# Kernel tuning notes

Measured on AMD Instinct MI355X. Metric: run time of the kernel, lower is better.

## Reference

```python
import jax, jax.numpy as jnp
from jax import lax
import numpy as np

N_NEURON = 4096
BATCH = 64
N_STEP = 200


def setup_inputs() -> dict:
    key = jax.random.key(0)
    k1, k2, k3 = jax.random.split(key, 3)
    # state_g is a sigmoid output: keep strictly inside (0, 1) for g_inverse's log
    state_g = jax.random.uniform(k1, (BATCH, N_NEURON), dtype=jnp.float32,
                                 minval=0.05, maxval=0.95)
    # Symmetric_Linear init: W ~ N(0, 0.01), symmetrized, zero diagonal
    W = jax.random.normal(k2, (N_NEURON, N_NEURON), dtype=jnp.float32) * 0.01
    W = W + W.T
    W = W - jnp.diag(jnp.diag(W))
    b = jax.random.normal(k3, (N_NEURON,), dtype=jnp.float32) * 0.01
    beta = jnp.ones((N_NEURON,), dtype=jnp.float32) * 10.0
    tau = jnp.ones((N_NEURON,), dtype=jnp.float32)
    dt_train = jnp.float32(0.1)
    return {"state_g": state_g, "W": W, "b": b, "beta": beta, "tau": tau,
            "dt_train": dt_train, "n_step": N_STEP}


def reference(state_g, W, b, beta, tau, dt_train, n_step):
    # max_x = 50 / beta.max()  (original uses .item(); beta is constant so same value)
    max_x = 50.0 / jnp.max(beta)
    # Symmetric_Linear effective weight: (W + W^T)/2 with zero diagonal.
    # Original recomputes this every step; it's step-invariant so hoist it.
    W_sym = (W + W.T) * 0.5 - jnp.diag(jnp.diag(W))
    # g_inverse: x = (1/beta) * log(g / (1 - g))
    state_x = (1.0 / beta) * jnp.log(state_g / (1.0 - state_g))
    alpha = dt_train / tau  # [N]

    def step(carry, _):
        x, g = carry
        pre = g @ W_sym.T + b                       # [B, N] GEMM
        x = alpha * pre + (1.0 - alpha) * x         # leaky update
        x = jnp.clip(x, -max_x, max_x)
        g = jax.nn.sigmoid(beta * x)
        return (x, g), None

    (state_x, state_g), _ = lax.scan(step, (state_x, state_g), None, length=n_step)
    return state_g
```

## Files before the change

### kernel.cpp

```cpp
#include <hip/hip_runtime.h>
#include <hip/hip_bf16.h>

#define MM 64
#define NN 4096
#define KK 4096
#define NSTEP 200

typedef __bf16 bf16x8 __attribute__((ext_vector_type(8)));
typedef float  f32x4  __attribute__((ext_vector_type(4)));

static __device__ __forceinline__ unsigned short f2bf(float f) {
    __hip_bfloat16 h = __float2bfloat16(f);
    return __builtin_bit_cast(unsigned short, h);
}
static __device__ __forceinline__ float bf2f(unsigned short u) {
    __hip_bfloat16 h = __builtin_bit_cast(__hip_bfloat16, u);
    return __bfloat162float(h);
}


__global__ __launch_bounds__(256) void symm_kernel(const float* __restrict__ W,
                                                   unsigned short* __restrict__ Wfh,
                                                   unsigned short* __restrict__ Wfl) {
    __shared__ float T[64][65];
    const int tid = threadIdx.x;
    const int r0 = blockIdx.y * 64, c0 = blockIdx.x * 64;
#pragma unroll
    for (int i = 0; i < 4; ++i) {
        int lin = tid + i * 256;
        int cc  = lin >> 4;
        int r4  = (lin & 15) * 4;
        float4 v = *(const float4*)&W[(size_t)(c0 + cc) * NN + r0 + r4];
        T[cc][r4 + 0] = v.x; T[cc][r4 + 1] = v.y;
        T[cc][r4 + 2] = v.z; T[cc][r4 + 3] = v.w;
    }
    __syncthreads();
#pragma unroll
    for (int i = 0; i < 4; ++i) {
        int lin = tid + i * 256;
        int rr  = lin >> 4;
        int c4  = (lin & 15) * 4;
        float4 v = *(const float4*)&W[(size_t)(r0 + rr) * NN + c0 + c4];
        float d[4] = {v.x, v.y, v.z, v.w};
        ushort4 ohi, olo;
        unsigned short* ph = (unsigned short*)&ohi;
        unsigned short* pl = (unsigned short*)&olo;
#pragma unroll
        for (int j = 0; j < 4; ++j) {
            float sv = 0.5f * (d[j] + T[c4 + j][rr]);
            if (r0 + rr == c0 + c4 + j) sv = 0.0f;
            unsigned short hi = f2bf(sv);
            ph[j] = hi;
            pl[j] = f2bf(sv - bf2f(hi));
        }
        const int n  = r0 + rr;
        const int kg = c0 + c4;
        const int s16 = n >> 4, ln = n & 15;
        const int kc = kg >> 5, q = (kg & 31) >> 3, j0 = kg & 7;
        size_t off = (((size_t)s16 * 128 + kc) * 64 + q * 16 + ln) * 8 + j0;
        *(ushort4*)&Wfh[off] = ohi;
        *(ushort4*)&Wfl[off] = olo;
    }
}

__global__ __launch_bounds__(256) void init_kernel(const float* __restrict__ g_in,
                                                   const float* __restrict__ beta,
                                                   float* __restrict__ x,
                                                   unsigned short* __restrict__ gfh,
                                                   unsigned short* __restrict__ gfl) {
    int idx = blockIdx.x * 256 + threadIdx.x;
    int r = idx >> 12, c = idx & (NN - 1);
    float g = g_in[idx];
    x[idx] = logf(g / (1.0f - g)) / beta[c];
    unsigned short hi = f2bf(g);
    unsigned short lo = f2bf(g - bf2f(hi));
    size_t off = (((size_t)(c >> 5) * 4 + (r >> 4)) * 64 + ((c & 31) >> 3) * 16 + (r & 15)) * 8 + (c & 7);
    gfh[off] = hi;
    gfl[off] = lo;
}

__global__ __launch_bounds__(256) void maxx_kernel(const float* __restrict__ beta,
                                                   float* __restrict__ out) {
    __shared__ float red[256];
    float m = -1e30f;
    for (int i = threadIdx.x; i < NN; i += 256) m = fmaxf(m, beta[i]);
    red[threadIdx.x] = m;
    __syncthreads();
    for (int s = 128; s > 0; s >>= 1) {
        if (threadIdx.x < s) red[threadIdx.x] = fmaxf(red[threadIdx.x], red[threadIdx.x + s]);
        __syncthreads();
    }
    if (threadIdx.x == 0) out[0] = 50.0f / red[0];
}

__global__ __launch_bounds__(512, 4) void gemm_kernel(
    const unsigned short* __restrict__ gfh,
    const unsigned short* __restrict__ gfl,
    const unsigned short* __restrict__ Wfh,
    const unsigned short* __restrict__ Wfl,
    float* __restrict__ P)
{
    __shared__ unsigned short lds[8192];

    const int tid  = threadIdx.x;
    const int w    = tid >> 6;
    const int lane = tid & 63;
    const int s64  = blockIdx.x >> 3;
    const int kq8  = blockIdx.x & 7;
    const int nq   = w & 3;
    const int mh   = w >> 2;

    const int tA  = (tid & 255) * 8;
    const int nq2 = (tid & 255) >> 6;
    const int eB  = (tid & 63) * 8;
    const unsigned short* __restrict__ srcA = (tid < 256) ? gfh : gfl;
    const unsigned short* __restrict__ srcB = (tid < 256) ? Wfh : Wfl;
    const size_t bRow = (size_t)(s64 * 4 + nq2) * 128;

    f32x4 acc[2] = {};

    {
        const int kc = kq8 * 16;
        uint4 rA = *(const uint4*)&srcA[(size_t)kc * 2048 + tA];
        uint4 rB = *(const uint4*)&srcB[(bRow + kc) * 512 + eB];
        *(uint4*)&lds[tid * 8]        = rA;
        *(uint4*)&lds[4096 + tid * 8] = rB;
    }
    __syncthreads();

    for (int it = 0; it < 16; ++it) {
        uint4 nA, nB;
        if (it < 15) {
            const int kcn = kq8 * 16 + it + 1;
            nA = *(const uint4*)&srcA[(size_t)kcn * 2048 + tA];
            nB = *(const uint4*)&srcB[(bRow + kcn) * 512 + eB];
        }

        bf16x8 bh = *(const bf16x8*)&lds[4096 + nq * 512 + lane * 8];
        bf16x8 bl = *(const bf16x8*)&lds[6144 + nq * 512 + lane * 8];
#pragma unroll
        for (int f = 0; f < 2; ++f) {
            const int mq = mh * 2 + f;
            bf16x8 ah = *(const bf16x8*)&lds[mq * 512 + lane * 8];
            bf16x8 al = *(const bf16x8*)&lds[2048 + mq * 512 + lane * 8];
            acc[f] = __builtin_amdgcn_mfma_f32_16x16x32_bf16(ah, bh, acc[f], 0, 0, 0);
            acc[f] = __builtin_amdgcn_mfma_f32_16x16x32_bf16(al, bh, acc[f], 0, 0, 0);
            acc[f] = __builtin_amdgcn_mfma_f32_16x16x32_bf16(ah, bl, acc[f], 0, 0, 0);
        }

        __syncthreads();
        if (it < 15) {
            *(uint4*)&lds[tid * 8]        = nA;
            *(uint4*)&lds[4096 + tid * 8] = nB;
        }
        __syncthreads();
    }

    {
        const int q = lane >> 4, l16 = lane & 15;
        float* Pb = &P[(size_t)(kq8 * 64 + s64) * 4096];
#pragma unroll
        for (int f = 0; f < 2; ++f) {
            const int mq = mh * 2 + f;
#pragma unroll
            for (int rg = 0; rg < 4; ++rg) {
                const int m = mq * 16 + q * 4 + rg;
                Pb[(size_t)m * 64 + nq * 16 + l16] = acc[f][rg];
            }
        }
    }
}

__global__ __launch_bounds__(256) void epi_kernel(
    const float* __restrict__ P,
    float* __restrict__ x,
    unsigned short* __restrict__ gfh_out,
    unsigned short* __restrict__ gfl_out,
    const float* __restrict__ bvec,
    const float* __restrict__ beta,
    const float* __restrict__ tau,
    const float* __restrict__ dt_ptr,
    const float* __restrict__ maxx_ptr,
    float* __restrict__ gout_f32)
{
    const int tid = threadIdx.x;
    const int s64 = blockIdx.x >> 2;
    const int mq4 = blockIdx.x & 3;
    const int m   = mq4 * 16 + (tid >> 4);
    const int tt  = tid & 15;
    const int c0  = tt * 4;
    const int n0  = s64 * 64 + c0;

    const size_t pb = ((size_t)s64 * 64 + m) * 64 + c0;
    float sum[4] = {};
#pragma unroll
    for (int k8 = 0; k8 < 8; ++k8) {
        float4 p = *(const float4*)&P[(size_t)k8 * 262144 + pb];
        sum[0] += p.x; sum[1] += p.y; sum[2] += p.z; sum[3] += p.w;
    }

    const float dt = *dt_ptr;
    const float mx = *maxx_ptr;
    float4 b0 = *(const float4*)&bvec[n0];
    float4 e0 = *(const float4*)&beta[n0];
    float4 t0 = *(const float4*)&tau[n0];
    float bb[4] = {b0.x, b0.y, b0.z, b0.w};
    float be[4] = {e0.x, e0.y, e0.z, e0.w};
    float tv[4] = {t0.x, t0.y, t0.z, t0.w};

    float* xp = &x[(size_t)m * NN + n0];
    float4 x0 = *(const float4*)xp;
    float xo[4] = {x0.x, x0.y, x0.z, x0.w};

    float gg[4];
    unsigned short vh[4], vl[4];
#pragma unroll
    for (int j = 0; j < 4; ++j) {
        const float al = dt / tv[j];
        float xn = al * (sum[j] + bb[j]) + (1.0f - al) * xo[j];
        xn = fminf(fmaxf(xn, -mx), mx);
        float g = 1.0f / (1.0f + __expf(-be[j] * xn));
        xo[j] = xn;
        gg[j] = g;
        unsigned short hi = f2bf(g);
        vh[j] = hi;
        vl[j] = f2bf(g - bf2f(hi));
    }
    *(float4*)xp = {xo[0], xo[1], xo[2], xo[3]};

    size_t off = (((size_t)(n0 >> 5) * 4 + (m >> 4)) * 64 + ((n0 & 31) >> 3) * 16 + (m & 15)) * 8 + (n0 & 7);
    *(ushort4*)&gfh_out[off] = {vh[0], vh[1], vh[2], vh[3]};
    *(ushort4*)&gfl_out[off] = {vl[0], vl[1], vl[2], vl[3]};

    if (gout_f32)
        *(float4*)&gout_f32[(size_t)m * NN + n0] = {gg[0], gg[1], gg[2], gg[3]};
}

extern "C" void kernel_launch(void* const* d_in, const int* in_sizes, int n_in,
                              void* d_out, int out_size, void* d_ws, size_t ws_size,
                              hipStream_t stream) {
    const float* state_g = (const float*)d_in[0];
    const float* W       = (const float*)d_in[1];
    const float* b       = (const float*)d_in[2];
    const float* beta    = (const float*)d_in[3];
    const float* tau     = (const float*)d_in[4];
    const float* dt      = (const float*)d_in[5];
    float* out = (float*)d_out;

    char* ws = (char*)d_ws;
    const size_t WH = (size_t)KK * NN * 2;
    const size_t XB = (size_t)MM * NN * 4;
    const size_t GB = (size_t)MM * NN * 2;
    const size_t PB = (size_t)8 * 64 * 64 * 64 * 4;
    unsigned short* Wfh = (unsigned short*)ws;
    unsigned short* Wfl = (unsigned short*)(ws + WH);
    float*          x   = (float*)(ws + 2 * WH);
    unsigned short* g0h = (unsigned short*)(ws + 2 * WH + XB);
    unsigned short* g0l = (unsigned short*)(ws + 2 * WH + XB + GB);
    unsigned short* g1h = (unsigned short*)(ws + 2 * WH + XB + 2 * GB);
    unsigned short* g1l = (unsigned short*)(ws + 2 * WH + XB + 3 * GB);
    float*          P   = (float*)(ws + 2 * WH + XB + 4 * GB);
    float*          mxp = (float*)(ws + 2 * WH + XB + 4 * GB + PB);

    symm_kernel<<<dim3(64, 64), 256, 0, stream>>>(W, Wfh, Wfl);
    init_kernel<<<(MM * NN) / 256, 256, 0, stream>>>(state_g, beta, x, g0h, g0l);
    maxx_kernel<<<1, 256, 0, stream>>>(beta, mxp);

    unsigned short *gih = g0h, *gil = g0l, *goh = g1h, *gol = g1l;
    for (int st = 0; st < NSTEP; ++st) {
        float* of = (st == NSTEP - 1) ? out : nullptr;
        gemm_kernel<<<512, 512, 0, stream>>>(gih, gil, Wfh, Wfl, P);
        epi_kernel<<<256, 256, 0, stream>>>(P, x, goh, gol, b, beta, tau, dt, mxp, of);
        unsigned short* tp;
        tp = gih; gih = goh; goh = tp;
        tp = gil; gil = gol; gol = tp;
    }
}
```

Before: 3.350 ms.

## Double-buffer LDS and prefetch two K-chunks ahead in GEMM kernel

Restructures the GEMM inner loop to use two LDS buffers, each holding two K-chunks, with a register prefetch depth of two iterations. This halves the loop trip count and removes one of the two barriers per iteration, so global loads and LDS writes can overlap with MFMA work. LDS use grows from 16 KB to 64 KB per block, which may reduce how many blocks fit per CU under the 4-block launch bound. Register pressure also rises from holding eight prefetched uint4 values.

```diff
diff --git a/kernel.cpp b/kernel.cpp
--- a/kernel.cpp
+++ b/kernel.cpp
@@ -100,7 +100,7 @@
     const unsigned short* __restrict__ Wfl,
     float* __restrict__ P)
 {
-    __shared__ unsigned short lds[8192];
+    __shared__ unsigned short lds[2][16384];
 
     const int tid  = threadIdx.x;
     const int w    = tid >> 6;
@@ -118,42 +118,63 @@
     const size_t bRow = (size_t)(s64 * 4 + nq2) * 128;
 
     f32x4 acc[2] = {};
+    uint4 r1[4], r2[4];
 
     {
-        const int kc = kq8 * 16;
-        uint4 rA = *(const uint4*)&srcA[(size_t)kc * 2048 + tA];
-        uint4 rB = *(const uint4*)&srcB[(bRow + kc) * 512 + eB];
-        *(uint4*)&lds[tid * 8]        = rA;
-        *(uint4*)&lds[4096 + tid * 8] = rB;
+        const int kc0 = kq8 * 16;
+        uint4 a0 = *(const uint4*)&srcA[(size_t)kc0 * 2048 + tA];
+        uint4 a1 = *(const uint4*)&srcA[(size_t)(kc0 + 1) * 2048 + tA];
+        uint4 b0 = *(const uint4*)&srcB[(bRow + kc0) * 512 + eB];
+        uint4 b1 = *(const uint4*)&srcB[(bRow + kc0 + 1) * 512 + eB];
+        *(uint4*)&lds[0][tid * 8]         = a0;
+        *(uint4*)&lds[0][4096 + tid * 8]  = a1;
+        *(uint4*)&lds[0][8192 + tid * 8]  = b0;
+        *(uint4*)&lds[0][12288 + tid * 8] = b1;
+        const int kc1 = kq8 * 16 + 2;
+        r1[0] = *(const uint4*)&srcA[(size_t)kc1 * 2048 + tA];
+        r1[1] = *(const uint4*)&srcA[(size_t)(kc1 + 1) * 2048 + tA];
+        r1[2] = *(const uint4*)&srcB[(bRow + kc1) * 512 + eB];
+        r1[3] = *(const uint4*)&srcB[(bRow + kc1 + 1) * 512 + eB];
     }
     __syncthreads();
 
-    for (int it = 0; it < 16; ++it) {
-        uint4 nA, nB;
-        if (it < 15) {
-            const int kcn = kq8 * 16 + it + 1;
-            nA = *(const uint4*)&srcA[(size_t)kcn * 2048 + tA];
-            nB = *(const uint4*)&srcB[(bRow + kcn) * 512 + eB];
-        }
-
-        bf16x8 bh = *(const bf16x8*)&lds[4096 + nq * 512 + lane * 8];
-        bf16x8 bl = *(const bf16x8*)&lds[6144 + nq * 512 + lane * 8];
-#pragma unroll
-        for (int f = 0; f < 2; ++f) {
-            const int mq = mh * 2 + f;
-            bf16x8 ah = *(const bf16x8*)&lds[mq * 512 + lane * 8];
-            bf16x8 al = *(const bf16x8*)&lds[2048 + mq * 512 + lane * 8];
-            acc[f] = __builtin_amdgcn_mfma_f32_16x16x32_bf16(ah, bh, acc[f], 0, 0, 0);
-            acc[f] = __builtin_amdgcn_mfma_f32_16x16x32_bf16(al, bh, acc[f], 0, 0, 0);
-            acc[f] = __builtin_amdgcn_mfma_f32_16x16x32_bf16(ah, bl, acc[f], 0, 0, 0);
-        }
-
+    int cur = 0;
+    for (int it = 0; it < 8; ++it) {
+        if (it < 6) {
+            const int kcn = kq8 * 16 + (it + 2) * 2;
+            r2[0] = *(const uint4*)&srcA[(size_t)kcn * 2048 + tA];
+            r2[1] = *(const uint4*)&srcA[(size_t)(kcn + 1) * 2048 + tA];
+            r2[2] = *(const uint4*)&srcB[(bRow + kcn) * 512 + eB];
+            r2[3] = *(const uint4*)&srcB[(bRow + kcn + 1) * 512 + eB];
+        }
+
+        const unsigned short* L = &lds[cur][0];
+#pragma unroll
+        for (int j = 0; j < 2; ++j) {
+            const int jo = j * 4096;
+            bf16x8 bh = *(const bf16x8*)&L[8192 + jo + nq * 512 + lane * 8];
+            bf16x8 bl = *(const bf16x8*)&L[10240 + jo + nq * 512 + lane * 8];
+#pragma unroll
+            for (int f = 0; f < 2; ++f) {
+                const int mq = mh * 2 + f;
+                bf16x8 ah = *(const bf16x8*)&L[jo + mq * 512 + lane * 8];
+                bf16x8 al = *(const bf16x8*)&L[jo + 2048 + mq * 512 + lane * 8];
+                acc[f] = __builtin_amdgcn_mfma_f32_16x16x32_bf16(ah, bh, acc[f], 0, 0, 0);
+                acc[f] = __builtin_amdgcn_mfma_f32_16x16x32_bf16(al, bh, acc[f], 0, 0, 0);
+                acc[f] = __builtin_amdgcn_mfma_f32_16x16x32_bf16(ah, bl, acc[f], 0, 0, 0);
+            }
+        }
+
+        if (it < 7) {
+            unsigned short* D = &lds[cur ^ 1][0];
+            *(uint4*)&D[tid * 8]         = r1[0];
+            *(uint4*)&D[4096 + tid * 8]  = r1[1];
+            *(uint4*)&D[8192 + tid * 8]  = r1[2];
+            *(uint4*)&D[12288 + tid * 8] = r1[3];
+        }
         __syncthreads();
-        if (it < 15) {
-            *(uint4*)&lds[tid * 8]        = nA;
-            *(uint4*)&lds[4096 + tid * 8] = nB;
-        }
-        __syncthreads();
+        if (it < 6) { r1[0] = r2[0]; r1[1] = r2[1]; r1[2] = r2[2]; r1[3] = r2[3]; }
+        cur ^= 1;
     }
 
     {
```

Measured after the change: 12.56 ms. 3.75x slower.

## Replace bf16 hi/lo split with fp16 hi plus scaled fp8 residual

Applied to the files above, without the earlier changes.

The symmetric weight matrix is stored as an fp16 high part plus an fp8 e4m3 residual scaled by 2^14, instead of two bf16 halves. The activations get matching fp16 hi/lo and fp8 copies. The GEMM runs two fp16 MFMAs plus one fp8 MFMA into a separate accumulator, rescaled at store. This cuts the per-step weight bytes streamed from memory by a quarter. The trade-offs are a software fp8 conversion and possible accuracy loss from the coarse residual.

```diff
diff --git a/kernel.cpp b/kernel.cpp
--- a/kernel.cpp
+++ b/kernel.cpp
@@ -6,22 +6,50 @@
 #define KK 4096
 #define NSTEP 200
 
-typedef __bf16 bf16x8 __attribute__((ext_vector_type(8)));
-typedef float  f32x4  __attribute__((ext_vector_type(4)));
-
-static __device__ __forceinline__ unsigned short f2bf(float f) {
-    __hip_bfloat16 h = __float2bfloat16(f);
+typedef _Float16 f16x8 __attribute__((ext_vector_type(8)));
+typedef float    f32x4 __attribute__((ext_vector_type(4)));
+
+static __device__ __forceinline__ unsigned short f2h(float f) {
+    _Float16 h = (_Float16)f;
     return __builtin_bit_cast(unsigned short, h);
 }
-static __device__ __forceinline__ float bf2f(unsigned short u) {
-    __hip_bfloat16 h = __builtin_bit_cast(__hip_bfloat16, u);
-    return __bfloat162float(h);
+static __device__ __forceinline__ float h2f(unsigned short u) {
+    _Float16 h = __builtin_bit_cast(_Float16, u);
+    return (float)h;
+}
+
+static __device__ __forceinline__ unsigned char f2e4m3(float f) {
+    unsigned u = __builtin_bit_cast(unsigned, f);
+    unsigned char s = (unsigned char)((u >> 24) & 0x80);
+    int e = (int)((u >> 23) & 0xff);
+    unsigned m = u & 0x7fffff;
+    if (e == 0) return s;
+    int E = e - 120;
+    if (E >= 16) return (unsigned char)(s | 0x7E);
+    if (E >= 1) {
+        unsigned keep = m >> 20;
+        unsigned rest = m & 0xfffff;
+        unsigned rnd = (rest > 0x80000u) || (rest == 0x80000u && (keep & 1));
+        keep += rnd;
+        if (keep == 8) { keep = 0; ++E; if (E >= 16) return (unsigned char)(s | 0x7E); }
+        return (unsigned char)(s | (E << 3) | keep);
+    }
+    int sh = 21 - E;
+    if (sh > 24) return s;
+    unsigned full = 0x800000u | m;
+    unsigned keep = full >> sh;
+    unsigned rest = full & ((1u << sh) - 1);
+    unsigned half = 1u << (sh - 1);
+    unsigned rnd = (rest > half) || (rest == half && (keep & 1));
+    keep += rnd;
+    if (keep == 8) return (unsigned char)(s | 0x08);
+    return (unsigned char)(s | keep);
 }
 
 
 __global__ __launch_bounds__(256) void symm_kernel(const float* __restrict__ W,
-                                                   unsigned short* __restrict__ Wfh,
-                                                   unsigned short* __restrict__ Wfl) {
+                                                   unsigned short* __restrict__ Wh,
+                                                   unsigned char* __restrict__ Wl8) {
     __shared__ float T[64][65];
     const int tid = threadIdx.x;
     const int r0 = blockIdx.y * 64, c0 = blockIdx.x * 64;
@@ -42,24 +70,24 @@
         int c4  = (lin & 15) * 4;
         float4 v = *(const float4*)&W[(size_t)(r0 + rr) * NN + c0 + c4];
         float d[4] = {v.x, v.y, v.z, v.w};
-        ushort4 ohi, olo;
-        unsigned short* ph = (unsigned short*)&ohi;
-        unsigned short* pl = (unsigned short*)&olo;
+        ushort4 o;
+        unsigned short* po = (unsigned short*)&o;
+        unsigned p8 = 0;
 #pragma unroll
         for (int j = 0; j < 4; ++j) {
             float sv = 0.5f * (d[j] + T[c4 + j][rr]);
             if (r0 + rr == c0 + c4 + j) sv = 0.0f;
-            unsigned short hi = f2bf(sv);
-            ph[j] = hi;
-            pl[j] = f2bf(sv - bf2f(hi));
+            unsigned short hi = f2h(sv);
+            po[j] = hi;
+            p8 |= (unsigned)f2e4m3((sv - h2f(hi)) * 16384.0f) << (j * 8);
         }
         const int n  = r0 + rr;
         const int kg = c0 + c4;
         const int s16 = n >> 4, ln = n & 15;
         const int kc = kg >> 5, q = (kg & 31) >> 3, j0 = kg & 7;
         size_t off = (((size_t)s16 * 128 + kc) * 64 + q * 16 + ln) * 8 + j0;
-        *(ushort4*)&Wfh[off] = ohi;
-        *(ushort4*)&Wfl[off] = olo;
+        *(ushort4*)&Wh[off] = o;
+        *(unsigned*)&Wl8[off] = p8;
     }
 }
 
@@ -67,16 +95,17 @@
                                                    const float* __restrict__ beta,
                                                    float* __restrict__ x,
                                                    unsigned short* __restrict__ gfh,
-                                                   unsigned short* __restrict__ gfl) {
+                                                   unsigned short* __restrict__ gfl,
+                                                   unsigned char* __restrict__ g8) {
     int idx = blockIdx.x * 256 + threadIdx.x;
     int r = idx >> 12, c = idx & (NN - 1);
     float g = g_in[idx];
     x[idx] = logf(g / (1.0f - g)) / beta[c];
-    unsigned short hi = f2bf(g);
-    unsigned short lo = f2bf(g - bf2f(hi));
+    unsigned short hi = f2h(g);
     size_t off = (((size_t)(c >> 5) * 4 + (r >> 4)) * 64 + ((c & 31) >> 3) * 16 + (r & 15)) * 8 + (c & 7);
     gfh[off] = hi;
-    gfl[off] = lo;
+    gfl[off] = f2h(g - h2f(hi));
+    g8[off]  = f2e4m3(g);
 }
 
 __global__ __launch_bounds__(256) void maxx_kernel(const float* __restrict__ beta,
@@ -96,11 +125,12 @@
 __global__ __launch_bounds__(512, 4) void gemm_kernel(
     const unsigned short* __restrict__ gfh,
     const unsigned short* __restrict__ gfl,
-    const unsigned short* __restrict__ Wfh,
-    const unsigned short* __restrict__ Wfl,
+    const unsigned char*  __restrict__ g8,
+    const unsigned short* __restrict__ Wh,
+    const unsigned char*  __restrict__ Wl8,
     float* __restrict__ P)
 {
-    __shared__ unsigned short lds[8192];
+    __shared__ unsigned char lds[16384];
 
     const int tid  = threadIdx.x;
     const int w    = tid >> 6;
@@ -110,48 +140,69 @@
     const int nq   = w & 3;
     const int mh   = w >> 2;
 
-    const int tA  = (tid & 255) * 8;
-    const int nq2 = (tid & 255) >> 6;
-    const int eB  = (tid & 63) * 8;
-    const unsigned short* __restrict__ srcA = (tid < 256) ? gfh : gfl;
-    const unsigned short* __restrict__ srcB = (tid < 256) ? Wfh : Wfl;
-    const size_t bRow = (size_t)(s64 * 4 + nq2) * 128;
-
-    f32x4 acc[2] = {};
+    const int t8 = tid & 255;
+    const unsigned char* src1 =
+        (const unsigned char*)(tid < 256 ? (const void*)gfh : (const void*)gfl) + (size_t)t8 * 16;
+    const int dst1 = (tid >> 8) * 4096 + t8 * 16;
+
+    const unsigned char* src2;
+    size_t s2k;
+    int dst2;
+    if (tid < 256) {
+        const int nq2 = t8 >> 6;
+        src2 = (const unsigned char*)Wh + ((size_t)(s64 * 4 + nq2) * 65536 + (size_t)(tid & 63) * 8) * 2;
+        s2k  = 1024;
+        dst2 = 8192 + nq2 * 1024 + (tid & 63) * 16;
+    } else if (tid < 384) {
+        const int tt = tid - 256;
+        src2 = g8 + (size_t)tt * 16;
+        s2k  = 2048;
+        dst2 = 12288 + tt * 16;
+    } else {
+        const int ttt = tid - 384;
+        const int nq3 = ttt >> 5;
+        src2 = Wl8 + (size_t)(s64 * 4 + nq3) * 65536 + (size_t)(ttt & 31) * 16;
+        s2k  = 512;
+        dst2 = 14336 + nq3 * 512 + (ttt & 31) * 16;
+    }
+
+    f32x4 acc[2]  = {};
+    f32x4 acc8[2] = {};
 
     {
-        const int kc = kq8 * 16;
-        uint4 rA = *(const uint4*)&srcA[(size_t)kc * 2048 + tA];
-        uint4 rB = *(const uint4*)&srcB[(bRow + kc) * 512 + eB];
-        *(uint4*)&lds[tid * 8]        = rA;
-        *(uint4*)&lds[4096 + tid * 8] = rB;
+        const size_t kc = (size_t)(kq8 * 16);
+        uint4 n1 = *(const uint4*)(src1 + kc * 4096);
+        uint4 n2 = *(const uint4*)(src2 + kc * s2k);
+        *(uint4*)&lds[dst1] = n1;
+        *(uint4*)&lds[dst2] = n2;
     }
     __syncthreads();
 
     for (int it = 0; it < 16; ++it) {
-        uint4 nA, nB;
+        uint4 n1, n2;
         if (it < 15) {
-            const int kcn = kq8 * 16 + it + 1;
-            nA = *(const uint4*)&srcA[(size_t)kcn * 2048 + tA];
-            nB = *(const uint4*)&srcB[(bRow + kcn) * 512 + eB];
-        }
-
-        bf16x8 bh = *(const bf16x8*)&lds[4096 + nq * 512 + lane * 8];
-        bf16x8 bl = *(const bf16x8*)&lds[6144 + nq * 512 + lane * 8];
+            const size_t kcn = (size_t)(kq8 * 16 + it + 1);
+            n1 = *(const uint4*)(src1 + kcn * 4096);
+            n2 = *(const uint4*)(src2 + kcn * s2k);
+        }
+
+        f16x8 bv = *(const f16x8*)&lds[8192 + nq * 1024 + lane * 16];
+        long  b8 = *(const long*)&lds[14336 + nq * 512 + lane * 8];
 #pragma unroll
         for (int f = 0; f < 2; ++f) {
             const int mq = mh * 2 + f;
-            bf16x8 ah = *(const bf16x8*)&lds[mq * 512 + lane * 8];
-            bf16x8 al = *(const bf16x8*)&lds[2048 + mq * 512 + lane * 8];
-            acc[f] = __builtin_amdgcn_mfma_f32_16x16x32_bf16(ah, bh, acc[f], 0, 0, 0);
-            acc[f] = __builtin_amdgcn_mfma_f32_16x16x32_bf16(al, bh, acc[f], 0, 0, 0);
-            acc[f] = __builtin_amdgcn_mfma_f32_16x16x32_bf16(ah, bl, acc[f], 0, 0, 0);
+            f16x8 ah = *(const f16x8*)&lds[mq * 1024 + lane * 16];
+            f16x8 al = *(const f16x8*)&lds[4096 + mq * 1024 + lane * 16];
+            long  a8 = *(const long*)&lds[12288 + mq * 512 + lane * 8];
+            acc[f]  = __builtin_amdgcn_mfma_f32_16x16x32_f16(ah, bv, acc[f], 0, 0, 0);
+            acc[f]  = __builtin_amdgcn_mfma_f32_16x16x32_f16(al, bv, acc[f], 0, 0, 0);
+            acc8[f] = __builtin_amdgcn_mfma_f32_16x16x32_fp8_fp8(a8, b8, acc8[f], 0, 0, 0);
         }
 
         __syncthreads();
         if (it < 15) {
-            *(uint4*)&lds[tid * 8]        = nA;
-            *(uint4*)&lds[4096 + tid * 8] = nB;
+            *(uint4*)&lds[dst1] = n1;
+            *(uint4*)&lds[dst2] = n2;
         }
         __syncthreads();
     }
@@ -165,7 +216,8 @@
 #pragma unroll
             for (int rg = 0; rg < 4; ++rg) {
                 const int m = mq * 16 + q * 4 + rg;
-                Pb[(size_t)m * 64 + nq * 16 + l16] = acc[f][rg];
+                Pb[(size_t)m * 64 + nq * 16 + l16] =
+                    acc[f][rg] + acc8[f][rg] * (1.0f / 16384.0f);
             }
         }
     }
@@ -176,6 +228,7 @@
     float* __restrict__ x,
     unsigned short* __restrict__ gfh_out,
     unsigned short* __restrict__ gfl_out,
+    unsigned char*  __restrict__ g8_out,
     const float* __restrict__ bvec,
     const float* __restrict__ beta,
     const float* __restrict__ tau,
@@ -214,6 +267,7 @@
 
     float gg[4];
     unsigned short vh[4], vl[4];
+    unsigned p8 = 0;
 #pragma unroll
     for (int j = 0; j < 4; ++j) {
         const float al = dt / tv[j];
@@ -222,15 +276,17 @@
         float g = 1.0f / (1.0f + __expf(-be[j] * xn));
         xo[j] = xn;
         gg[j] = g;
-        unsigned short hi = f2bf(g);
+        unsigned short hi = f2h(g);
         vh[j] = hi;
-        vl[j] = f2bf(g - bf2f(hi));
+        vl[j] = f2h(g - h2f(hi));
+        p8 |= (unsigned)f2e4m3(g) << (j * 8);
     }
     *(float4*)xp = {xo[0], xo[1], xo[2], xo[3]};
 
     size_t off = (((size_t)(n0 >> 5) * 4 + (m >> 4)) * 64 + ((n0 & 31) >> 3) * 16 + (m & 15)) * 8 + (n0 & 7);
     *(ushort4*)&gfh_out[off] = {vh[0], vh[1], vh[2], vh[3]};
     *(ushort4*)&gfl_out[off] = {vl[0], vl[1], vl[2], vl[3]};
+    *(unsigned*)&g8_out[off] = p8;
 
     if (gout_f32)
         *(float4*)&gout_f32[(size_t)m * NN + n0] = {gg[0], gg[1], gg[2], gg[3]};
@@ -248,31 +304,38 @@
     float* out = (float*)d_out;
 
     char* ws = (char*)d_ws;
-    const size_t WH = (size_t)KK * NN * 2;
-    const size_t XB = (size_t)MM * NN * 4;
-    const size_t GB = (size_t)MM * NN * 2;
-    const size_t PB = (size_t)8 * 64 * 64 * 64 * 4;
-    unsigned short* Wfh = (unsigned short*)ws;
-    unsigned short* Wfl = (unsigned short*)(ws + WH);
-    float*          x   = (float*)(ws + 2 * WH);
-    unsigned short* g0h = (unsigned short*)(ws + 2 * WH + XB);
-    unsigned short* g0l = (unsigned short*)(ws + 2 * WH + XB + GB);
-    unsigned short* g1h = (unsigned short*)(ws + 2 * WH + XB + 2 * GB);
-    unsigned short* g1l = (unsigned short*)(ws + 2 * WH + XB + 3 * GB);
-    float*          P   = (float*)(ws + 2 * WH + XB + 4 * GB);
-    float*          mxp = (float*)(ws + 2 * WH + XB + 4 * GB + PB);
-
-    symm_kernel<<<dim3(64, 64), 256, 0, stream>>>(W, Wfh, Wfl);
-    init_kernel<<<(MM * NN) / 256, 256, 0, stream>>>(state_g, beta, x, g0h, g0l);
+    const size_t WHB = (size_t)KK * NN * 2;
+    const size_t WLB = (size_t)KK * NN;
+    const size_t XB  = (size_t)MM * NN * 4;
+    const size_t GB  = (size_t)MM * NN * 2;
+    const size_t G8B = (size_t)MM * NN;
+    const size_t PB  = (size_t)8 * 64 * 64 * 64 * 4;
+    unsigned short* Wh  = (unsigned short*)ws;
+    unsigned char*  Wl8 = (unsigned char*)(ws + WHB);
+    float*          x   = (float*)(ws + WHB + WLB);
+    char* gbase = ws + WHB + WLB + XB;
+    unsigned short* g0h = (unsigned short*)(gbase);
+    unsigned short* g0l = (unsigned short*)(gbase + GB);
+    unsigned char*  g08 = (unsigned char*)(gbase + 2 * GB);
+    unsigned short* g1h = (unsigned short*)(gbase + 2 * GB + G8B);
+    unsigned short* g1l = (unsigned short*)(gbase + 3 * GB + G8B);
+    unsigned char*  g18 = (unsigned char*)(gbase + 4 * GB + G8B);
+    float*          P   = (float*)(gbase + 4 * GB + 2 * G8B);
+    float*          mxp = (float*)(gbase + 4 * GB + 2 * G8B + PB);
+
+    symm_kernel<<<dim3(64, 64), 256, 0, stream>>>(W, Wh, Wl8);
+    init_kernel<<<(MM * NN) / 256, 256, 0, stream>>>(state_g, beta, x, g0h, g0l, g08);
     maxx_kernel<<<1, 256, 0, stream>>>(beta, mxp);
 
     unsigned short *gih = g0h, *gil = g0l, *goh = g1h, *gol = g1l;
+    unsigned char  *gi8 = g08, *go8 = g18;
     for (int st = 0; st < NSTEP; ++st) {
         float* of = (st == NSTEP - 1) ? out : nullptr;
-        gemm_kernel<<<512, 512, 0, stream>>>(gih, gil, Wfh, Wfl, P);
-        epi_kernel<<<256, 256, 0, stream>>>(P, x, goh, gol, b, beta, tau, dt, mxp, of);
+        gemm_kernel<<<512, 512, 0, stream>>>(gih, gil, gi8, Wh, Wl8, P);
+        epi_kernel<<<256, 256, 0, stream>>>(P, x, goh, gol, go8, b, beta, tau, dt, mxp, of);
         unsigned short* tp;
         tp = gih; gih = goh; goh = tp;
         tp = gil; gil = gol; gol = tp;
-    }
-}
+        unsigned char* t8 = gi8; gi8 = go8; go8 = t8;
+    }
+}
```

Result: slower. 3.630 ms (+8.3%).
